# Kernel tuning notes

Hardware: AMD Instinct MI355X
Metric: run time of the kernel (lower is better)

The kernel has to match this reference:

```python
import jax, jax.numpy as jnp
import numpy as np

B, T, V, D, H, C = 128, 512, 50000, 128, 256, 10


def _lstm_scan(xs, W, U, b):
    # xs: [T, B, in]; Keras gate order i, f, g(candidate), o.
    xW = jnp.einsum('tbi,ij->tbj', xs, W) + b  # precompute input projection
    Bsz = xs.shape[1]
    Hd = U.shape[0]
    h0 = jnp.zeros((Bsz, Hd), xs.dtype)

    def step(carry, zx):
        h, c = carry
        z = zx + h @ U
        i, f, g, o = jnp.split(z, 4, axis=-1)
        i = jax.nn.sigmoid(i)
        f = jax.nn.sigmoid(f)
        g = jnp.tanh(g)
        o = jax.nn.sigmoid(o)
        c = f * c + i * g
        h = o * jnp.tanh(c)
        return (h, c), h

    (hT, _), hs = jax.lax.scan(step, (h0, h0), xW)
    return hs, hT


def setup_inputs() -> dict:
    key = jax.random.key(0)
    ks = jax.random.split(key, 16)
    f32 = jnp.float32

    def glorot(k, shape):
        fan = shape[0] + shape[1]
        return jax.random.uniform(k, shape, f32, -1.0, 1.0) * np.sqrt(6.0 / fan)

    x = jax.random.randint(ks[0], (B, T), 0, V, dtype=jnp.int32)
    emb = jax.random.normal(ks[1], (V, D), f32) * 0.05
    # layer 1: input D -> 4H per direction
    W1f = glorot(ks[2], (D, 4 * H)); U1f = glorot(ks[3], (H, 4 * H)); b1f = jnp.zeros((4 * H,), f32)
    W1b = glorot(ks[4], (D, 4 * H)); U1b = glorot(ks[5], (H, 4 * H)); b1b = jnp.zeros((4 * H,), f32)
    # layer 2: input 2H -> 4H per direction
    W2f = glorot(ks[6], (2 * H, 4 * H)); U2f = glorot(ks[7], (H, 4 * H)); b2f = jnp.zeros((4 * H,), f32)
    W2b = glorot(ks[8], (2 * H, 4 * H)); U2b = glorot(ks[9], (H, 4 * H)); b2b = jnp.zeros((4 * H,), f32)
    Wd = glorot(ks[10], (2 * H, C)); bd = jnp.zeros((C,), f32)
    return dict(x=x, emb=emb, W1f=W1f, U1f=U1f, b1f=b1f, W1b=W1b, U1b=U1b, b1b=b1b,
                W2f=W2f, U2f=U2f, b2f=b2f, W2b=W2b, U2b=U2b, b2b=b2b, Wd=Wd, bd=bd)


def reference(x, emb, W1f, U1f, b1f, W1b, U1b, b1b, W2f, U2f, b2f, W2b, U2b, b2b, Wd, bd):
    # Embedding lookup -> [T, B, D] (time-major for scan). Dropout is inference-off.
    e = jnp.transpose(emb[x], (1, 0, 2))
    # Bidirectional LSTM 1 (return_sequences)
    hs_f, _ = _lstm_scan(e, W1f, U1f, b1f)
    hs_b, _ = _lstm_scan(e[::-1], W1b, U1b, b1b)
    seq = jnp.concatenate([hs_f, hs_b[::-1]], axis=-1)  # [T, B, 2H]
    # Bidirectional LSTM 2 (return last states)
    _, hT_f = _lstm_scan(seq, W2f, U2f, b2f)
    _, hT_b = _lstm_scan(seq[::-1], W2b, U2b, b2b)
    h = jnp.concatenate([hT_f, hT_b], axis=-1)  # [B, 2H]
    return jax.nn.softmax(h @ Wd + bd, axis=-1)
```

## Files before the change

kernel.cpp:

```cpp
#include <hip/hip_runtime.h>
#include <hip/hip_bf16.h>

#define B_ 128
#define T_ 512
#define H_ 256
#define G4_ 1024
#define D_ 128

typedef short s8v   __attribute__((ext_vector_type(8)));
typedef float f32x4 __attribute__((ext_vector_type(4)));
typedef unsigned short u16x4 __attribute__((ext_vector_type(4)));
typedef unsigned short u16x8 __attribute__((ext_vector_type(8)));
typedef unsigned int   u32x4 __attribute__((ext_vector_type(4)));
typedef unsigned short ush;
typedef unsigned long long ull;

__device__ __align__(256) ush   g_xw[(size_t)T_ * 2 * B_ * G4_];
__device__ __align__(256) ush   g_hseq[(size_t)T_ * B_ * 512];
__device__ __align__(256) ull   g_hx2[8 * 2 * 2 * 256 * 8];
__device__ __align__(256) float g_hT[B_ * 512];
__device__ __align__(256) ush   g_wtall[2359296];

__device__ __forceinline__ ush f2b(float f) {
  unsigned u = __builtin_bit_cast(unsigned, f);
  u += 0x7FFFu + ((u >> 16) & 1u);
  return (ush)(u >> 16);
}
__device__ __forceinline__ float b2f(ush h) {
  unsigned u = ((unsigned)h) << 16;
  return __builtin_bit_cast(float, u);
}
__device__ __forceinline__ float sigm(float x) {
  x = fminf(15.f, fmaxf(-15.f, x));
  return 1.f / (1.f + __expf(-x));
}
__device__ __forceinline__ float tanh_(float x) {
  x = fminf(8.f, fmaxf(-8.f, x));
  float e = __expf(-2.f * x);
  return (1.f - e) / (1.f + e);
}

__global__ __launch_bounds__(256, 4) void prep_w(
    const float* __restrict__ Wf, const float* __restrict__ Wb,
    ush* __restrict__ WTf, ush* __restrict__ WTb, int K)
{
  __shared__ ush tile[64][65];
  const float* W = blockIdx.z ? Wb : Wf;
  ush* WT = blockIdx.z ? WTb : WTf;
  int nt = blockIdx.x & 15, kt = blockIdx.x >> 4;
  int tid = threadIdx.x;
  for (int i = tid; i < 4096; i += 256) {
    int k = i >> 6, n = i & 63;
    tile[k][n] = f2b(W[(size_t)(kt * 64 + k) * 1024 + nt * 64 + n]);
  }
  __syncthreads();
  for (int i = tid; i < 4096; i += 256) {
    int n = i >> 6, k = i & 63;
    WT[(size_t)(nt * 64 + n) * K + kt * 64 + k] = tile[k][n];
  }
}

__global__ __launch_bounds__(512, 4) void gemm_xw(
    int mode, const int* __restrict__ xi, const float* __restrict__ emb,
    const ush* __restrict__ WTf, const ush* __restrict__ WTb, int ktot)
{
  __shared__ __align__(16) ush A_lds[128 * 72];
  __shared__ __align__(16) ush BT_lds[128 * 72];
  const int tid = threadIdx.x;
  const int lane = tid & 63;
  const int w = tid >> 6;
  const int nb = blockIdx.x;
  const int t = blockIdx.y;
  const int dir = blockIdx.z;
  const ush* WT = dir ? WTb : WTf;

  const f32x4 zero4 = {0.f, 0.f, 0.f, 0.f};
  f32x4 acc[8];
#pragma unroll
  for (int i = 0; i < 8; ++i) acc[i] = zero4;

  const int rowA0 = tid >> 3;
  const int ccA = tid & 7;
  int idx0 = 0, idx1 = 0;
  if (mode == 0) {
    idx0 = xi[rowA0 * T_ + t];
    idx1 = xi[(rowA0 + 64) * T_ + t];
  }

  const int nch = ktot >> 6;
  for (int kc = 0; kc < nch; ++kc) {
    __syncthreads();
    if (mode == 0) {
      {
        const float* s = emb + (size_t)idx0 * D_ + kc * 64 + ccA * 8;
        f32x4 a = *(const f32x4*)s;
        f32x4 b = *(const f32x4*)(s + 4);
        u16x8 v;
        v[0]=f2b(a[0]); v[1]=f2b(a[1]); v[2]=f2b(a[2]); v[3]=f2b(a[3]);
        v[4]=f2b(b[0]); v[5]=f2b(b[1]); v[6]=f2b(b[2]); v[7]=f2b(b[3]);
        *(u16x8*)&A_lds[rowA0 * 72 + ccA * 8] = v;
      }
      {
        const float* s = emb + (size_t)idx1 * D_ + kc * 64 + ccA * 8;
        f32x4 a = *(const f32x4*)s;
        f32x4 b = *(const f32x4*)(s + 4);
        u16x8 v;
        v[0]=f2b(a[0]); v[1]=f2b(a[1]); v[2]=f2b(a[2]); v[3]=f2b(a[3]);
        v[4]=f2b(b[0]); v[5]=f2b(b[1]); v[6]=f2b(b[2]); v[7]=f2b(b[3]);
        *(u16x8*)&A_lds[(rowA0 + 64) * 72 + ccA * 8] = v;
      }
    } else {
      {
        const ush* s = g_hseq + ((size_t)(t * B_ + rowA0)) * 512 + kc * 64 + ccA * 8;
        *(u32x4*)&A_lds[rowA0 * 72 + ccA * 8] = *(const u32x4*)s;
      }
      {
        const ush* s = g_hseq + ((size_t)(t * B_ + rowA0 + 64)) * 512 + kc * 64 + ccA * 8;
        *(u32x4*)&A_lds[(rowA0 + 64) * 72 + ccA * 8] = *(const u32x4*)s;
      }
    }
    {
      int n = tid >> 2, k8 = (tid & 3) * 2;
      const ush* src = WT + (size_t)(nb * 128 + n) * ktot + kc * 64 + k8 * 8;
      *(u32x4*)&BT_lds[n * 72 + k8 * 8] = *(const u32x4*)src;
      *(u32x4*)&BT_lds[n * 72 + k8 * 8 + 8] = *(const u32x4*)(src + 8);
    }
    __syncthreads();
#pragma unroll
    for (int kt = 0; kt < 2; ++kt) {
      const int koff = kt * 32 + ((lane >> 4) << 3);
      s8v af = *(const s8v*)&A_lds[(w * 16 + (lane & 15)) * 72 + koff];
#pragma unroll
      for (int nt = 0; nt < 8; ++nt) {
        s8v bf = *(const s8v*)&BT_lds[(nt * 16 + (lane & 15)) * 72 + koff];
        acc[nt] = __builtin_amdgcn_mfma_f32_16x16x32_bf16(af, bf, acc[nt], 0, 0, 0);
      }
    }
  }
  ush* dst = g_xw + ((size_t)t * 2 + dir) * ((size_t)B_ * G4_);
#pragma unroll
  for (int nt = 0; nt < 8; ++nt) {
    int colg = nb * 128 + nt * 16 + (lane & 15);
    int g = colg >> 8, hc = colg & 255;
#pragma unroll
    for (int jj = 0; jj < 4; ++jj) {
      int row = w * 16 + ((lane >> 4) << 2) + jj;
      dst[(size_t)row * 1024 + hc * 4 + g] = f2b(acc[nt][jj]);
    }
  }
}

__global__ __launch_bounds__(512, 2) void lstm_rec(
    int layer, const ush* __restrict__ UTf, const ush* __restrict__ UTb,
    const float* __restrict__ bfp, const float* __restrict__ bbp,
    int writeSeq)
{
  __shared__ __align__(16) ush h_lds[2][16 * 256];

  const int tid = threadIdx.x;
  const int lane = tid & 63;
  const int w = tid >> 6;
  const int dir = blockIdx.x >> 4;
  const int nh = (blockIdx.x >> 3) & 1;
  const int slice = blockIdx.x & 7;
  const ush* UT = dir ? UTb : UTf;
  const float* bias = dir ? bbp : bfp;

  const int l15 = lane & 15;
  const int lq = lane >> 4;
  const int mycol = nh * 128 + w * 16 + l15;
  const int rowb = slice * 16;
  const unsigned sbase = (unsigned)(layer * T_);

  s8v bfr[4][8];
#pragma unroll
  for (int g = 0; g < 4; ++g) {
    const ush* up = UT + (size_t)(g * 256 + mycol) * 256;
#pragma unroll
    for (int kt = 0; kt < 8; ++kt)
      bfr[g][kt] = *(const s8v*)(up + kt * 32 + lq * 8);
  }
  float bias_r[4];
#pragma unroll
  for (int g = 0; g < 4; ++g) bias_r[g] = bias[g * 256 + mycol];

  {
    ull* z = (ull*)&h_lds[0][0];
    for (int i = tid; i < 1024; i += 512) z[i] = 0ull;
  }
  __syncthreads();

  float c_[4] = {0.f, 0.f, 0.f, 0.f};
  ull* hxp = g_hx2 + ((size_t)(slice * 2 + dir) * 2) * (256 * 8);

  const int colp = (nh ^ 1) * 128 + (tid >> 2);
  const int q = tid & 3;
  const int c8p = colp >> 3, wp = colp & 7;

  u16x4 xv[4];
  {
    int t0 = dir ? (T_ - 1) : 0;
    const ush* xp = g_xw + (((size_t)t0 * 2 + dir) * B_ + rowb) * 1024 + mycol * 4;
#pragma unroll
    for (int j = 0; j < 4; ++j)
      xv[j] = *(const u16x4*)(xp + (size_t)(lq * 4 + j) * 1024);
  }

  for (int s = 0; s < T_; ++s) {
    const int p = s & 1;

    if (s > 0) {
      const ull* a0 = hxp + ((size_t)p * 256 + colp) * 8 + q * 2;
      unsigned target = sbase + (unsigned)s;
      ull v0, v1;
      for (;;) {
        v0 = __hip_atomic_load(a0, __ATOMIC_RELAXED, __HIP_MEMORY_SCOPE_SYSTEM);
        v1 = __hip_atomic_load(a0 + 1, __ATOMIC_RELAXED, __HIP_MEMORY_SCOPE_SYSTEM);
        if ((unsigned)(v0 >> 32) >= target && (unsigned)(v1 >> 32) >= target) break;
        __builtin_amdgcn_s_sleep(1);
      }
      ush* dstl = &h_lds[p][0];
      dstl[(q * 4 + 0) * 256 + (((c8p ^ (q * 4 + 0)) & 31) * 8 + wp)] = (ush)v0;
      dstl[(q * 4 + 1) * 256 + (((c8p ^ (q * 4 + 1)) & 31) * 8 + wp)] = (ush)(v0 >> 16);
      dstl[(q * 4 + 2) * 256 + (((c8p ^ (q * 4 + 2)) & 31) * 8 + wp)] = (ush)v1;
      dstl[(q * 4 + 3) * 256 + (((c8p ^ (q * 4 + 3)) & 31) * 8 + wp)] = (ush)(v1 >> 16);
    }
    __syncthreads();

    if (writeSeq && s > 0 && tid < 256) {
      int row = tid >> 4, idx = tid & 15;
      int col = nh * 128 + idx * 8;
      int c8 = col >> 3;
      u32x4 hval = *(const u32x4*)&h_lds[p][row * 256 + ((c8 ^ row) & 31) * 8];
      int tprev = dir ? (T_ - s) : (s - 1);
      *(u32x4*)&g_hseq[((size_t)tprev * B_ + rowb + row) * 512 + dir * 256 + col] = hval;
    }

    s8v af[8];
#pragma unroll
    for (int kt = 0; kt < 8; ++kt) {
      int c8 = kt * 4 + lq;
      af[kt] = *(const s8v*)&h_lds[p][l15 * 256 + ((c8 ^ l15) & 31) * 8];
    }
    f32x4 acc[4];
    const f32x4 zero4 = {0.f, 0.f, 0.f, 0.f};
#pragma unroll
    for (int g = 0; g < 4; ++g) acc[g] = zero4;
#pragma unroll
    for (int kt = 0; kt < 8; ++kt) {
#pragma unroll
      for (int g = 0; g < 4; ++g)
        acc[g] = __builtin_amdgcn_mfma_f32_16x16x32_bf16(af[kt], bfr[g][kt], acc[g], 0, 0, 0);
    }
    float hf[4];
    ush hv[4];
#pragma unroll
    for (int j = 0; j < 4; ++j) {
      float vi = acc[0][j] + b2f(xv[j][0]) + bias_r[0];
      float vf = acc[1][j] + b2f(xv[j][1]) + bias_r[1];
      float vg = acc[2][j] + b2f(xv[j][2]) + bias_r[2];
      float vo = acc[3][j] + b2f(xv[j][3]) + bias_r[3];
      float ig = sigm(vi), fg = sigm(vf), gg = tanh_(vg), og = sigm(vo);
      float cc = fg * c_[j] + ig * gg;
      c_[j] = cc;
      hf[j] = og * tanh_(cc);
      hv[j] = f2b(hf[j]);
    }
    {
      ull seqw = ((ull)(sbase + (unsigned)s + 1u)) << 32;
      ull e0 = (ull)hv[0] | ((ull)hv[1] << 16) | seqw;
      ull e1 = (ull)hv[2] | ((ull)hv[3] << 16) | seqw;
      ull* ep = hxp + ((size_t)(p ^ 1) * 256 + mycol) * 8 + lq * 2;
      __hip_atomic_store(ep, e0, __ATOMIC_RELAXED, __HIP_MEMORY_SCOPE_SYSTEM);
      __hip_atomic_store(ep + 1, e1, __ATOMIC_RELAXED, __HIP_MEMORY_SCOPE_SYSTEM);
    }
    {
      int c8o = mycol >> 3, wo = mycol & 7;
#pragma unroll
      for (int j = 0; j < 4; ++j) {
        int row = lq * 4 + j;
        h_lds[p ^ 1][row * 256 + (((c8o ^ row) & 31) * 8 + wo)] = hv[j];
      }
    }
    if (s + 1 < T_) {
      int tn = dir ? (T_ - 2 - s) : (s + 1);
      const ush* xp = g_xw + (((size_t)tn * 2 + dir) * B_ + rowb) * 1024 + mycol * 4;
#pragma unroll
      for (int j = 0; j < 4; ++j)
        xv[j] = *(const u16x4*)(xp + (size_t)(lq * 4 + j) * 1024);
    }
  }

  {
    const ull* a0 = hxp + ((size_t)(T_ & 1) * 256 + colp) * 8 + q * 2;
    unsigned target = sbase + (unsigned)T_;
    ull v0, v1;
    for (;;) {
      v0 = __hip_atomic_load(a0, __ATOMIC_RELAXED, __HIP_MEMORY_SCOPE_SYSTEM);
      v1 = __hip_atomic_load(a0 + 1, __ATOMIC_RELAXED, __HIP_MEMORY_SCOPE_SYSTEM);
      if ((unsigned)(v0 >> 32) >= target && (unsigned)(v1 >> 32) >= target) break;
      __builtin_amdgcn_s_sleep(1);
    }
    ush* dstl = &h_lds[T_ & 1][0];
    dstl[(q * 4 + 0) * 256 + (((c8p ^ (q * 4 + 0)) & 31) * 8 + wp)] = (ush)v0;
    dstl[(q * 4 + 1) * 256 + (((c8p ^ (q * 4 + 1)) & 31) * 8 + wp)] = (ush)(v0 >> 16);
    dstl[(q * 4 + 2) * 256 + (((c8p ^ (q * 4 + 2)) & 31) * 8 + wp)] = (ush)v1;
    dstl[(q * 4 + 3) * 256 + (((c8p ^ (q * 4 + 3)) & 31) * 8 + wp)] = (ush)(v1 >> 16);
  }
  __syncthreads();
  if (tid < 256) {
    int row = tid >> 4, idx = tid & 15;
    int col = nh * 128 + idx * 8;
    int c8 = col >> 3;
    u32x4 hval = *(const u32x4*)&h_lds[T_ & 1][row * 256 + ((c8 ^ row) & 31) * 8];
    if (writeSeq) {
      int tprev = dir ? 0 : (T_ - 1);
      *(u32x4*)&g_hseq[((size_t)tprev * B_ + rowb + row) * 512 + dir * 256 + col] = hval;
    } else {
      const ush* hp = (const ush*)&hval;
      float* dstf = g_hT + (size_t)(rowb + row) * 512 + dir * 256 + col;
      f32x4 f0, f1;
#pragma unroll
      for (int j = 0; j < 4; ++j) { f0[j] = b2f(hp[j]); f1[j] = b2f(hp[4 + j]); }
      *(f32x4*)dstf = f0;
      *(f32x4*)(dstf + 4) = f1;
    }
  }
}

__global__ __launch_bounds__(512, 1) void dense_softmax(
    const float* __restrict__ Wd, const float* __restrict__ bd, float* __restrict__ out)
{
  __shared__ float wT[10 * 512];
  __shared__ float part[512 * 10];
  int tid = threadIdx.x;
  for (int i = tid; i < 5120; i += 512) {
    int k = i / 10, j = i - k * 10;
    wT[j * 512 + k] = Wd[i];
  }
  __syncthreads();
  int row = tid >> 2, q = tid & 3;
  float acc[10];
#pragma unroll
  for (int j = 0; j < 10; ++j) acc[j] = 0.f;
  const float* hrow = g_hT + (size_t)row * 512 + q * 128;
  for (int kk = 0; kk < 32; ++kk) {
    f32x4 h4 = *(const f32x4*)(hrow + kk * 4);
#pragma unroll
    for (int j = 0; j < 10; ++j) {
      f32x4 w4 = *(const f32x4*)&wT[j * 512 + q * 128 + kk * 4];
      acc[j] += h4[0] * w4[0] + h4[1] * w4[1] + h4[2] * w4[2] + h4[3] * w4[3];
    }
  }
#pragma unroll
  for (int j = 0; j < 10; ++j) part[tid * 10 + j] = acc[j];
  __syncthreads();
  if (tid < 128) {
    float lg[10];
#pragma unroll
    for (int j = 0; j < 10; ++j)
      lg[j] = bd[j] + part[(tid * 4 + 0) * 10 + j] + part[(tid * 4 + 1) * 10 + j]
                    + part[(tid * 4 + 2) * 10 + j] + part[(tid * 4 + 3) * 10 + j];
    float m = lg[0];
#pragma unroll
    for (int j = 1; j < 10; ++j) m = fmaxf(m, lg[j]);
    float ssum = 0.f;
#pragma unroll
    for (int j = 0; j < 10; ++j) { lg[j] = __expf(lg[j] - m); ssum += lg[j]; }
    float inv = 1.f / ssum;
#pragma unroll
    for (int j = 0; j < 10; ++j) out[tid * 10 + j] = lg[j] * inv;
  }
}

extern "C" void kernel_launch(void* const* d_in, const int* in_sizes, int n_in,
                              void* d_out, int out_size, void* d_ws, size_t ws_size,
                              hipStream_t stream) {
  (void)in_sizes; (void)n_in; (void)d_ws; (void)ws_size; (void)out_size;
  const int* x = (const int*)d_in[0];
  const float* emb = (const float*)d_in[1];
  const float* W1f = (const float*)d_in[2];
  const float* U1f = (const float*)d_in[3];
  const float* b1f = (const float*)d_in[4];
  const float* W1b = (const float*)d_in[5];
  const float* U1b = (const float*)d_in[6];
  const float* b1b = (const float*)d_in[7];
  const float* W2f = (const float*)d_in[8];
  const float* U2f = (const float*)d_in[9];
  const float* b2f = (const float*)d_in[10];
  const float* W2b = (const float*)d_in[11];
  const float* U2b = (const float*)d_in[12];
  const float* b2b = (const float*)d_in[13];
  const float* Wd  = (const float*)d_in[14];
  const float* bd  = (const float*)d_in[15];
  float* out = (float*)d_out;

  void* hx_p = nullptr; void* wt_p = nullptr;
  hipGetSymbolAddress(&hx_p, HIP_SYMBOL(g_hx2));
  hipGetSymbolAddress(&wt_p, HIP_SYMBOL(g_wtall));
  ush* wt = (ush*)wt_p;
  hipMemsetAsync(hx_p, 0, sizeof(ull) * 8 * 2 * 2 * 256 * 8, stream);

  ush* wt1f = wt;                 ush* wt1b = wt1f + 131072;
  ush* ut1f = wt1b + 131072;      ush* ut1b = ut1f + 262144;
  ush* wt2f = ut1b + 262144;      ush* wt2b = wt2f + 524288;
  ush* ut2f = wt2b + 524288;      ush* ut2b = ut2f + 262144;

  prep_w<<<dim3(32, 1, 2), 256, 0, stream>>>(W1f, W1b, wt1f, wt1b, 128);
  prep_w<<<dim3(64, 1, 2), 256, 0, stream>>>(U1f, U1b, ut1f, ut1b, 256);
  prep_w<<<dim3(128, 1, 2), 256, 0, stream>>>(W2f, W2b, wt2f, wt2b, 512);
  prep_w<<<dim3(64, 1, 2), 256, 0, stream>>>(U2f, U2b, ut2f, ut2b, 256);

  gemm_xw<<<dim3(8, T_, 2), 512, 0, stream>>>(0, x, emb, wt1f, wt1b, 128);
  lstm_rec<<<32, 512, 0, stream>>>(0, ut1f, ut1b, b1f, b1b, 1);
  gemm_xw<<<dim3(8, T_, 2), 512, 0, stream>>>(1, nullptr, nullptr, wt2f, wt2b, 512);
  lstm_rec<<<32, 512, 0, stream>>>(1, ut2f, ut2b, b2f, b2b, 0);
  dense_softmax<<<1, 512, 0, stream>>>(Wd, bd, out);
}
```

Measured before the change: 3.872 ms.

## Fuse layer-2 input GEMM into layer-1 recurrence via per-timestep readiness counters

The layer-1 recurrent kernel becomes a persistent mega-kernel. 64 blocks run the LSTM recurrence, now split into 16 batch slices of 8 rows instead of 8 slices of 16, giving twice as many recurrent blocks. The remaining 160 blocks compute the layer-2 input projection GEMM as soon as per-timestep counters show both directions have written that timestep's hidden state. This hides the layer-2 xW GEMM under the latency-bound layer-1 scan and removes a separate kernel launch. In exchange it adds atomic counters, spin-waiting, and a co-residency assumption: GEMM blocks must not starve the recurrent blocks.

```diff
diff --git a/kernel.cpp b/kernel.cpp
--- a/kernel.cpp
+++ b/kernel.cpp
@@ -17,8 +17,9 @@
 
 __device__ __align__(256) ush   g_xw[(size_t)T_ * 2 * B_ * G4_];
 __device__ __align__(256) ush   g_hseq[(size_t)T_ * B_ * 512];
-__device__ __align__(256) ull   g_hx2[8 * 2 * 2 * 256 * 8];
+__device__ __align__(256) ull   g_hx2[16 * 2 * 2 * 256 * 4];
 __device__ __align__(256) float g_hT[B_ * 512];
+__device__ __align__(256) unsigned g_tcnt[512];
 __device__ __align__(256) ush   g_wtall[2359296];
 
 __device__ __forceinline__ ush f2b(float f) {
@@ -61,8 +62,8 @@
 }
 
 __global__ __launch_bounds__(512, 4) void gemm_xw(
-    int mode, const int* __restrict__ xi, const float* __restrict__ emb,
-    const ush* __restrict__ WTf, const ush* __restrict__ WTb, int ktot)
+    const int* __restrict__ xi, const float* __restrict__ emb,
+    const ush* __restrict__ WTf, const ush* __restrict__ WTb)
 {
   __shared__ __align__(16) ush A_lds[128 * 72];
   __shared__ __align__(16) ush BT_lds[128 * 72];
@@ -81,47 +82,32 @@
 
   const int rowA0 = tid >> 3;
   const int ccA = tid & 7;
-  int idx0 = 0, idx1 = 0;
-  if (mode == 0) {
-    idx0 = xi[rowA0 * T_ + t];
-    idx1 = xi[(rowA0 + 64) * T_ + t];
-  }
-
-  const int nch = ktot >> 6;
-  for (int kc = 0; kc < nch; ++kc) {
+  int idx0 = xi[rowA0 * T_ + t];
+  int idx1 = xi[(rowA0 + 64) * T_ + t];
+
+  for (int kc = 0; kc < 2; ++kc) {
     __syncthreads();
-    if (mode == 0) {
-      {
-        const float* s = emb + (size_t)idx0 * D_ + kc * 64 + ccA * 8;
-        f32x4 a = *(const f32x4*)s;
-        f32x4 b = *(const f32x4*)(s + 4);
-        u16x8 v;
-        v[0]=f2b(a[0]); v[1]=f2b(a[1]); v[2]=f2b(a[2]); v[3]=f2b(a[3]);
-        v[4]=f2b(b[0]); v[5]=f2b(b[1]); v[6]=f2b(b[2]); v[7]=f2b(b[3]);
-        *(u16x8*)&A_lds[rowA0 * 72 + ccA * 8] = v;
-      }
-      {
-        const float* s = emb + (size_t)idx1 * D_ + kc * 64 + ccA * 8;
-        f32x4 a = *(const f32x4*)s;
-        f32x4 b = *(const f32x4*)(s + 4);
-        u16x8 v;
-        v[0]=f2b(a[0]); v[1]=f2b(a[1]); v[2]=f2b(a[2]); v[3]=f2b(a[3]);
-        v[4]=f2b(b[0]); v[5]=f2b(b[1]); v[6]=f2b(b[2]); v[7]=f2b(b[3]);
-        *(u16x8*)&A_lds[(rowA0 + 64) * 72 + ccA * 8] = v;
-      }
-    } else {
-      {
-        const ush* s = g_hseq + ((size_t)(t * B_ + rowA0)) * 512 + kc * 64 + ccA * 8;
-        *(u32x4*)&A_lds[rowA0 * 72 + ccA * 8] = *(const u32x4*)s;
-      }
-      {
-        const ush* s = g_hseq + ((size_t)(t * B_ + rowA0 + 64)) * 512 + kc * 64 + ccA * 8;
-        *(u32x4*)&A_lds[(rowA0 + 64) * 72 + ccA * 8] = *(const u32x4*)s;
-      }
+    {
+      const float* s = emb + (size_t)idx0 * D_ + kc * 64 + ccA * 8;
+      f32x4 a = *(const f32x4*)s;
+      f32x4 b = *(const f32x4*)(s + 4);
+      u16x8 v;
+      v[0]=f2b(a[0]); v[1]=f2b(a[1]); v[2]=f2b(a[2]); v[3]=f2b(a[3]);
+      v[4]=f2b(b[0]); v[5]=f2b(b[1]); v[6]=f2b(b[2]); v[7]=f2b(b[3]);
+      *(u16x8*)&A_lds[rowA0 * 72 + ccA * 8] = v;
+    }
+    {
+      const float* s = emb + (size_t)idx1 * D_ + kc * 64 + ccA * 8;
+      f32x4 a = *(const f32x4*)s;
+      f32x4 b = *(const f32x4*)(s + 4);
+      u16x8 v;
+      v[0]=f2b(a[0]); v[1]=f2b(a[1]); v[2]=f2b(a[2]); v[3]=f2b(a[3]);
+      v[4]=f2b(b[0]); v[5]=f2b(b[1]); v[6]=f2b(b[2]); v[7]=f2b(b[3]);
+      *(u16x8*)&A_lds[(rowA0 + 64) * 72 + ccA * 8] = v;
     }
     {
       int n = tid >> 2, k8 = (tid & 3) * 2;
-      const ush* src = WT + (size_t)(nb * 128 + n) * ktot + kc * 64 + k8 * 8;
+      const ush* src = WT + (size_t)(nb * 128 + n) * 128 + kc * 64 + k8 * 8;
       *(u32x4*)&BT_lds[n * 72 + k8 * 8] = *(const u32x4*)src;
       *(u32x4*)&BT_lds[n * 72 + k8 * 8 + 8] = *(const u32x4*)(src + 8);
     }
@@ -150,180 +136,251 @@
   }
 }
 
-__global__ __launch_bounds__(512, 2) void lstm_rec(
+__global__ __launch_bounds__(512, 2) void mega(
     int layer, const ush* __restrict__ UTf, const ush* __restrict__ UTb,
     const float* __restrict__ bfp, const float* __restrict__ bbp,
-    int writeSeq)
+    int writeSeq, int ngemm,
+    const ush* __restrict__ WT2f, const ush* __restrict__ WT2b)
 {
-  __shared__ __align__(16) ush h_lds[2][16 * 256];
-
+  __shared__ __align__(16) ush smem[2 * 128 * 72];
+  const int bx = blockIdx.x;
   const int tid = threadIdx.x;
   const int lane = tid & 63;
   const int w = tid >> 6;
-  const int dir = blockIdx.x >> 4;
-  const int nh = (blockIdx.x >> 3) & 1;
-  const int slice = blockIdx.x & 7;
-  const ush* UT = dir ? UTb : UTf;
-  const float* bias = dir ? bbp : bfp;
-
   const int l15 = lane & 15;
   const int lq = lane >> 4;
-  const int mycol = nh * 128 + w * 16 + l15;
-  const int rowb = slice * 16;
-  const unsigned sbase = (unsigned)(layer * T_);
-
-  s8v bfr[4][8];
-#pragma unroll
-  for (int g = 0; g < 4; ++g) {
-    const ush* up = UT + (size_t)(g * 256 + mycol) * 256;
-#pragma unroll
-    for (int kt = 0; kt < 8; ++kt)
-      bfr[g][kt] = *(const s8v*)(up + kt * 32 + lq * 8);
-  }
-  float bias_r[4];
-#pragma unroll
-  for (int g = 0; g < 4; ++g) bias_r[g] = bias[g * 256 + mycol];
-
-  {
-    ull* z = (ull*)&h_lds[0][0];
-    for (int i = tid; i < 1024; i += 512) z[i] = 0ull;
-  }
-  __syncthreads();
-
-  float c_[4] = {0.f, 0.f, 0.f, 0.f};
-  ull* hxp = g_hx2 + ((size_t)(slice * 2 + dir) * 2) * (256 * 8);
-
-  const int colp = (nh ^ 1) * 128 + (tid >> 2);
-  const int q = tid & 3;
-  const int c8p = colp >> 3, wp = colp & 7;
-
-  u16x4 xv[4];
-  {
-    int t0 = dir ? (T_ - 1) : 0;
-    const ush* xp = g_xw + (((size_t)t0 * 2 + dir) * B_ + rowb) * 1024 + mycol * 4;
-#pragma unroll
-    for (int j = 0; j < 4; ++j)
-      xv[j] = *(const u16x4*)(xp + (size_t)(lq * 4 + j) * 1024);
-  }
-
-  for (int s = 0; s < T_; ++s) {
-    const int p = s & 1;
-
-    if (s > 0) {
-      const ull* a0 = hxp + ((size_t)p * 256 + colp) * 8 + q * 2;
-      unsigned target = sbase + (unsigned)s;
-      ull v0, v1;
+
+  if (bx < 64) {
+    const int slice = bx & 15;
+    const int dir = (bx >> 4) & 1;
+    const int nh = bx >> 5;
+    const ush* UT = dir ? UTb : UTf;
+    const float* bias = dir ? bbp : bfp;
+    const int mycol = nh * 128 + w * 16 + l15;
+    const int rowb = slice * 8;
+    const unsigned sbase = (unsigned)(layer * T_);
+    ush* h0 = smem;
+
+    s8v bfr[4][8];
+#pragma unroll
+    for (int g = 0; g < 4; ++g) {
+      const ush* up = UT + (size_t)(g * 256 + mycol) * 256;
+#pragma unroll
+      for (int kt = 0; kt < 8; ++kt)
+        bfr[g][kt] = *(const s8v*)(up + kt * 32 + lq * 8);
+    }
+    float bias_r[4];
+#pragma unroll
+    for (int g = 0; g < 4; ++g) bias_r[g] = bias[g * 256 + mycol];
+
+    {
+      ull* z = (ull*)smem;
+      z[tid] = 0ull; z[tid + 512] = 0ull; z[tid + 1024] = 0ull; z[tid + 1536] = 0ull;
+    }
+    __syncthreads();
+
+    float c_[4] = {0.f, 0.f, 0.f, 0.f};
+    ull* hx_base = g_hx2 + (size_t)(slice * 2 + dir) * 2048;
+    const int colp = (nh ^ 1) * 128 + (tid >> 2);
+    const int m_ = tid & 3;
+    const int c8p = colp >> 3, wp = colp & 7;
+    const int xrow = (lq & 1) * 4;
+
+    u16x4 xv[4];
+    {
+      int t0 = dir ? (T_ - 1) : 0;
+      const ush* xp = g_xw + (((size_t)t0 * 2 + dir) * B_ + rowb) * 1024 + mycol * 4;
+#pragma unroll
+      for (int j = 0; j < 4; ++j) xv[j] = *(const u16x4*)(xp + (size_t)(xrow + j) * 1024);
+    }
+
+    for (int s = 0; s < T_; ++s) {
+      const int p = s & 1;
+      if (s > 0) {
+        ull* aP = hx_base + ((size_t)p * 256 + colp) * 4 + m_;
+        unsigned target = sbase + (unsigned)s;
+        ull v;
+        for (;;) {
+          v = __hip_atomic_load(aP, __ATOMIC_RELAXED, __HIP_MEMORY_SCOPE_SYSTEM);
+          if ((unsigned)(v >> 32) >= target) break;
+          __builtin_amdgcn_s_sleep(1);
+        }
+        int r0 = 2 * m_;
+        ush* dl = h0 + p * 4096;
+        dl[r0 * 256 + (((c8p ^ r0) & 31) * 8 + wp)] = (ush)v;
+        dl[(r0 + 1) * 256 + (((c8p ^ (r0 + 1)) & 31) * 8 + wp)] = (ush)(v >> 16);
+      }
+      __syncthreads();
+      if (writeSeq) {
+        if (tid == 0 && s >= 2) {
+          int td = dir ? (T_ + 1 - s) : (s - 2);
+          __hip_atomic_fetch_add(&g_tcnt[td], 1u, __ATOMIC_RELAXED, __HIP_MEMORY_SCOPE_SYSTEM);
+        }
+        if (s > 0 && tid < 128) {
+          int row8 = tid >> 4, idx = tid & 15;
+          int col = nh * 128 + idx * 8;
+          int c8 = col >> 3;
+          const ush* srcl = h0 + p * 4096 + row8 * 256 + ((c8 ^ row8) & 31) * 8;
+          ull lo = *(const ull*)srcl;
+          ull hi = *(const ull*)(srcl + 4);
+          int tprev = dir ? (T_ - s) : (s - 1);
+          ull* dst = (ull*)&g_hseq[((size_t)tprev * B_ + rowb + row8) * 512 + dir * 256 + col];
+          __hip_atomic_store(dst, lo, __ATOMIC_RELAXED, __HIP_MEMORY_SCOPE_SYSTEM);
+          __hip_atomic_store(dst + 1, hi, __ATOMIC_RELAXED, __HIP_MEMORY_SCOPE_SYSTEM);
+        }
+      }
+      u16x4 xn[4];
+      if (s + 1 < T_) {
+        int tn = dir ? (T_ - 2 - s) : (s + 1);
+        const ush* xp = g_xw + (((size_t)tn * 2 + dir) * B_ + rowb) * 1024 + mycol * 4;
+#pragma unroll
+        for (int j = 0; j < 4; ++j) xn[j] = *(const u16x4*)(xp + (size_t)(xrow + j) * 1024);
+      }
+      s8v af[8];
+#pragma unroll
+      for (int kt = 0; kt < 8; ++kt) {
+        int c8 = kt * 4 + lq;
+        af[kt] = *(const s8v*)(h0 + p * 4096 + l15 * 256 + ((c8 ^ l15) & 31) * 8);
+      }
+      f32x4 acc[4];
+      const f32x4 zero4 = {0.f, 0.f, 0.f, 0.f};
+#pragma unroll
+      for (int g = 0; g < 4; ++g) acc[g] = zero4;
+#pragma unroll
+      for (int kt = 0; kt < 8; ++kt) {
+#pragma unroll
+        for (int g = 0; g < 4; ++g)
+          acc[g] = __builtin_amdgcn_mfma_f32_16x16x32_bf16(af[kt], bfr[g][kt], acc[g], 0, 0, 0);
+      }
+      float hf[4];
+      ush hv[4];
+#pragma unroll
+      for (int j = 0; j < 4; ++j) {
+        float vi = acc[0][j] + b2f(xv[j][0]) + bias_r[0];
+        float vf = acc[1][j] + b2f(xv[j][1]) + bias_r[1];
+        float vg = acc[2][j] + b2f(xv[j][2]) + bias_r[2];
+        float vo = acc[3][j] + b2f(xv[j][3]) + bias_r[3];
+        float ig = sigm(vi), fg = sigm(vf), gg = tanh_(vg), og = sigm(vo);
+        float cc = fg * c_[j] + ig * gg;
+        c_[j] = cc;
+        hf[j] = og * tanh_(cc);
+        hv[j] = f2b(hf[j]);
+      }
+      (void)hf;
+      if (lq < 2) {
+        ull seqw = ((ull)(sbase + (unsigned)s + 1u)) << 32;
+        ull e0 = (ull)hv[0] | ((ull)hv[1] << 16) | seqw;
+        ull e1 = (ull)hv[2] | ((ull)hv[3] << 16) | seqw;
+        ull* ep = hx_base + ((size_t)(p ^ 1) * 256 + mycol) * 4 + 2 * lq;
+        __hip_atomic_store(ep, e0, __ATOMIC_RELAXED, __HIP_MEMORY_SCOPE_SYSTEM);
+        __hip_atomic_store(ep + 1, e1, __ATOMIC_RELAXED, __HIP_MEMORY_SCOPE_SYSTEM);
+        int c8o = mycol >> 3, wo = mycol & 7;
+        ush* dl = h0 + (p ^ 1) * 4096;
+#pragma unroll
+        for (int j = 0; j < 4; ++j) {
+          int r = lq * 4 + j;
+          dl[r * 256 + (((c8o ^ r) & 31) * 8 + wo)] = hv[j];
+        }
+      }
+#pragma unroll
+      for (int j = 0; j < 4; ++j) xv[j] = xn[j];
+    }
+    __syncthreads();
+    const ush* bufl = h0 + (T_ & 1) * 4096;
+    if (writeSeq) {
+      if (tid < 128) {
+        int row8 = tid >> 4, idx = tid & 15;
+        int col = nh * 128 + idx * 8;
+        int c8 = col >> 3;
+        const ush* srcl = bufl + row8 * 256 + ((c8 ^ row8) & 31) * 8;
+        ull lo = *(const ull*)srcl;
+        ull hi = *(const ull*)(srcl + 4);
+        int tlast = dir ? 0 : (T_ - 1);
+        ull* dst = (ull*)&g_hseq[((size_t)tlast * B_ + rowb + row8) * 512 + dir * 256 + col];
+        __hip_atomic_store(dst, lo, __ATOMIC_RELAXED, __HIP_MEMORY_SCOPE_SYSTEM);
+        __hip_atomic_store(dst + 1, hi, __ATOMIC_RELAXED, __HIP_MEMORY_SCOPE_SYSTEM);
+      }
+      asm volatile("s_waitcnt vmcnt(0)" ::: "memory");
+      __syncthreads();
+      if (tid == 0) {
+        int ta = dir ? 1 : (T_ - 2);
+        int tb2 = dir ? 0 : (T_ - 1);
+        __hip_atomic_fetch_add(&g_tcnt[ta], 1u, __ATOMIC_RELAXED, __HIP_MEMORY_SCOPE_SYSTEM);
+        __hip_atomic_fetch_add(&g_tcnt[tb2], 1u, __ATOMIC_RELAXED, __HIP_MEMORY_SCOPE_SYSTEM);
+      }
+    } else {
+      if (tid < 128) {
+        int row8 = tid >> 4, idx = tid & 15;
+        int col = nh * 128 + idx * 8;
+        int c8 = col >> 3;
+        const ush* srcl = bufl + row8 * 256 + ((c8 ^ row8) & 31) * 8;
+        float* dstf = g_hT + (size_t)(rowb + row8) * 512 + dir * 256 + col;
+        f32x4 f0, f1;
+#pragma unroll
+        for (int j = 0; j < 4; ++j) { f0[j] = b2f(srcl[j]); f1[j] = b2f(srcl[4 + j]); }
+        *(f32x4*)dstf = f0;
+        *(f32x4*)(dstf + 4) = f1;
+      }
+    }
+  } else {
+    if (ngemm <= 0) return;
+    ush* A_lds = smem;
+    ush* BT_lds = smem + 128 * 72;
+    const int wg = bx - 64;
+    const int rowA0 = tid >> 3;
+    const int ccA = tid & 7;
+
+    for (int u = wg; u < 8192; u += ngemm) {
+      int pairIdx = u >> 4, sub = u & 15;
+      int nb = sub & 7, gdir = sub >> 3;
+      int t = (pairIdx & 1) ? (255 - (pairIdx >> 1)) : (256 + (pairIdx >> 1));
+      const ush* WT = gdir ? WT2b : WT2f;
       for (;;) {
-        v0 = __hip_atomic_load(a0, __ATOMIC_RELAXED, __HIP_MEMORY_SCOPE_SYSTEM);
-        v1 = __hip_atomic_load(a0 + 1, __ATOMIC_RELAXED, __HIP_MEMORY_SCOPE_SYSTEM);
-        if ((unsigned)(v0 >> 32) >= target && (unsigned)(v1 >> 32) >= target) break;
-        __builtin_amdgcn_s_sleep(1);
-      }
-      ush* dstl = &h_lds[p][0];
-      dstl[(q * 4 + 0) * 256 + (((c8p ^ (q * 4 + 0)) & 31) * 8 + wp)] = (ush)v0;
-      dstl[(q * 4 + 1) * 256 + (((c8p ^ (q * 4 + 1)) & 31) * 8 + wp)] = (ush)(v0 >> 16);
-      dstl[(q * 4 + 2) * 256 + (((c8p ^ (q * 4 + 2)) & 31) * 8 + wp)] = (ush)v1;
-      dstl[(q * 4 + 3) * 256 + (((c8p ^ (q * 4 + 3)) & 31) * 8 + wp)] = (ush)(v1 >> 16);
-    }
-    __syncthreads();
-
-    if (writeSeq && s > 0 && tid < 256) {
-      int row = tid >> 4, idx = tid & 15;
-      int col = nh * 128 + idx * 8;
-      int c8 = col >> 3;
-      u32x4 hval = *(const u32x4*)&h_lds[p][row * 256 + ((c8 ^ row) & 31) * 8];
-      int tprev = dir ? (T_ - s) : (s - 1);
-      *(u32x4*)&g_hseq[((size_t)tprev * B_ + rowb + row) * 512 + dir * 256 + col] = hval;
-    }
-
-    s8v af[8];
-#pragma unroll
-    for (int kt = 0; kt < 8; ++kt) {
-      int c8 = kt * 4 + lq;
-      af[kt] = *(const s8v*)&h_lds[p][l15 * 256 + ((c8 ^ l15) & 31) * 8];
-    }
-    f32x4 acc[4];
-    const f32x4 zero4 = {0.f, 0.f, 0.f, 0.f};
-#pragma unroll
-    for (int g = 0; g < 4; ++g) acc[g] = zero4;
-#pragma unroll
-    for (int kt = 0; kt < 8; ++kt) {
-#pragma unroll
-      for (int g = 0; g < 4; ++g)
-        acc[g] = __builtin_amdgcn_mfma_f32_16x16x32_bf16(af[kt], bfr[g][kt], acc[g], 0, 0, 0);
-    }
-    float hf[4];
-    ush hv[4];
-#pragma unroll
-    for (int j = 0; j < 4; ++j) {
-      float vi = acc[0][j] + b2f(xv[j][0]) + bias_r[0];
-      float vf = acc[1][j] + b2f(xv[j][1]) + bias_r[1];
-      float vg = acc[2][j] + b2f(xv[j][2]) + bias_r[2];
-      float vo = acc[3][j] + b2f(xv[j][3]) + bias_r[3];
-      float ig = sigm(vi), fg = sigm(vf), gg = tanh_(vg), og = sigm(vo);
-      float cc = fg * c_[j] + ig * gg;
-      c_[j] = cc;
-      hf[j] = og * tanh_(cc);
-      hv[j] = f2b(hf[j]);
-    }
-    {
-      ull seqw = ((ull)(sbase + (unsigned)s + 1u)) << 32;
-      ull e0 = (ull)hv[0] | ((ull)hv[1] << 16) | seqw;
-      ull e1 = (ull)hv[2] | ((ull)hv[3] << 16) | seqw;
-      ull* ep = hxp + ((size_t)(p ^ 1) * 256 + mycol) * 8 + lq * 2;
-      __hip_atomic_store(ep, e0, __ATOMIC_RELAXED, __HIP_MEMORY_SCOPE_SYSTEM);
-      __hip_atomic_store(ep + 1, e1, __ATOMIC_RELAXED, __HIP_MEMORY_SCOPE_SYSTEM);
-    }
-    {
-      int c8o = mycol >> 3, wo = mycol & 7;
-#pragma unroll
-      for (int j = 0; j < 4; ++j) {
-        int row = lq * 4 + j;
-        h_lds[p ^ 1][row * 256 + (((c8o ^ row) & 31) * 8 + wo)] = hv[j];
-      }
-    }
-    if (s + 1 < T_) {
-      int tn = dir ? (T_ - 2 - s) : (s + 1);
-      const ush* xp = g_xw + (((size_t)tn * 2 + dir) * B_ + rowb) * 1024 + mycol * 4;
-#pragma unroll
-      for (int j = 0; j < 4; ++j)
-        xv[j] = *(const u16x4*)(xp + (size_t)(lq * 4 + j) * 1024);
-    }
-  }
-
-  {
-    const ull* a0 = hxp + ((size_t)(T_ & 1) * 256 + colp) * 8 + q * 2;
-    unsigned target = sbase + (unsigned)T_;
-    ull v0, v1;
-    for (;;) {
-      v0 = __hip_atomic_load(a0, __ATOMIC_RELAXED, __HIP_MEMORY_SCOPE_SYSTEM);
-      v1 = __hip_atomic_load(a0 + 1, __ATOMIC_RELAXED, __HIP_MEMORY_SCOPE_SYSTEM);
-      if ((unsigned)(v0 >> 32) >= target && (unsigned)(v1 >> 32) >= target) break;
-      __builtin_amdgcn_s_sleep(1);
-    }
-    ush* dstl = &h_lds[T_ & 1][0];
-    dstl[(q * 4 + 0) * 256 + (((c8p ^ (q * 4 + 0)) & 31) * 8 + wp)] = (ush)v0;
-    dstl[(q * 4 + 1) * 256 + (((c8p ^ (q * 4 + 1)) & 31) * 8 + wp)] = (ush)(v0 >> 16);
-    dstl[(q * 4 + 2) * 256 + (((c8p ^ (q * 4 + 2)) & 31) * 8 + wp)] = (ush)v1;
-    dstl[(q * 4 + 3) * 256 + (((c8p ^ (q * 4 + 3)) & 31) * 8 + wp)] = (ush)(v1 >> 16);
-  }
-  __syncthreads();
-  if (tid < 256) {
-    int row = tid >> 4, idx = tid & 15;
-    int col = nh * 128 + idx * 8;
-    int c8 = col >> 3;
-    u32x4 hval = *(const u32x4*)&h_lds[T_ & 1][row * 256 + ((c8 ^ row) & 31) * 8];
-    if (writeSeq) {
-      int tprev = dir ? 0 : (T_ - 1);
-      *(u32x4*)&g_hseq[((size_t)tprev * B_ + rowb + row) * 512 + dir * 256 + col] = hval;
-    } else {
-      const ush* hp = (const ush*)&hval;
-      float* dstf = g_hT + (size_t)(rowb + row) * 512 + dir * 256 + col;
-      f32x4 f0, f1;
-#pragma unroll
-      for (int j = 0; j < 4; ++j) { f0[j] = b2f(hp[j]); f1[j] = b2f(hp[4 + j]); }
-      *(f32x4*)dstf = f0;
-      *(f32x4*)(dstf + 4) = f1;
+        unsigned v = __hip_atomic_load(&g_tcnt[t], __ATOMIC_RELAXED, __HIP_MEMORY_SCOPE_SYSTEM);
+        if (v >= 64u) break;
+        __builtin_amdgcn_s_sleep(4);
+      }
+      const f32x4 zero4 = {0.f, 0.f, 0.f, 0.f};
+      f32x4 acc[8];
+#pragma unroll
+      for (int i = 0; i < 8; ++i) acc[i] = zero4;
+      for (int kc = 0; kc < 8; ++kc) {
+        __syncthreads();
+        {
+          const ush* s0 = g_hseq + ((size_t)(t * B_ + rowA0)) * 512 + kc * 64 + ccA * 8;
+          *(u32x4*)&A_lds[rowA0 * 72 + ccA * 8] = *(const u32x4*)s0;
+          const ush* s1 = g_hseq + ((size_t)(t * B_ + rowA0 + 64)) * 512 + kc * 64 + ccA * 8;
+          *(u32x4*)&A_lds[(rowA0 + 64) * 72 + ccA * 8] = *(const u32x4*)s1;
+        }
+        {
+          int n = tid >> 2, k8 = (tid & 3) * 2;
+          const ush* src = WT + (size_t)(nb * 128 + n) * 512 + kc * 64 + k8 * 8;
+          *(u32x4*)&BT_lds[n * 72 + k8 * 8] = *(const u32x4*)src;
+          *(u32x4*)&BT_lds[n * 72 + k8 * 8 + 8] = *(const u32x4*)(src + 8);
+        }
+        __syncthreads();
+#pragma unroll
+        for (int kt = 0; kt < 2; ++kt) {
+          const int koff = kt * 32 + (lq << 3);
+          s8v af = *(const s8v*)&A_lds[(w * 16 + l15) * 72 + koff];
+#pragma unroll
+          for (int nt = 0; nt < 8; ++nt) {
+            s8v bf = *(const s8v*)&BT_lds[(nt * 16 + l15) * 72 + koff];
+            acc[nt] = __builtin_amdgcn_mfma_f32_16x16x32_bf16(af, bf, acc[nt], 0, 0, 0);
+          }
+        }
+      }
+      ush* dst = g_xw + ((size_t)t * 2 + gdir) * ((size_t)B_ * G4_);
+#pragma unroll
+      for (int nt = 0; nt < 8; ++nt) {
+        int colg = nb * 128 + nt * 16 + l15;
+        int g = colg >> 8, hc = colg & 255;
+#pragma unroll
+        for (int jj = 0; jj < 4; ++jj) {
+          int row = w * 16 + (lq << 2) + jj;
+          dst[(size_t)row * 1024 + hc * 4 + g] = f2b(acc[nt][jj]);
+        }
+      }
     }
   }
 }
@@ -395,11 +452,13 @@
   const float* bd  = (const float*)d_in[15];
   float* out = (float*)d_out;
 
-  void* hx_p = nullptr; void* wt_p = nullptr;
+  void* hx_p = nullptr; void* wt_p = nullptr; void* tc_p = nullptr;
   hipGetSymbolAddress(&hx_p, HIP_SYMBOL(g_hx2));
   hipGetSymbolAddress(&wt_p, HIP_SYMBOL(g_wtall));
+  hipGetSymbolAddress(&tc_p, HIP_SYMBOL(g_tcnt));
   ush* wt = (ush*)wt_p;
-  hipMemsetAsync(hx_p, 0, sizeof(ull) * 8 * 2 * 2 * 256 * 8, stream);
+  hipMemsetAsync(hx_p, 0, sizeof(ull) * 16 * 2 * 2 * 256 * 4, stream);
+  hipMemsetAsync(tc_p, 0, sizeof(unsigned) * 512, stream);
 
   ush* wt1f = wt;                 ush* wt1b = wt1f + 131072;
   ush* ut1f = wt1b + 131072;      ush* ut1b = ut1f + 262144;
@@ -411,9 +470,8 @@
   prep_w<<<dim3(128, 1, 2), 256, 0, stream>>>(W2f, W2b, wt2f, wt2b, 512);
   prep_w<<<dim3(64, 1, 2), 256, 0, stream>>>(U2f, U2b, ut2f, ut2b, 256);
 
-  gemm_xw<<<dim3(8, T_, 2), 512, 0, stream>>>(0, x, emb, wt1f, wt1b, 128);
-  lstm_rec<<<32, 512, 0, stream>>>(0, ut1f, ut1b, b1f, b1b, 1);
-  gemm_xw<<<dim3(8, T_, 2), 512, 0, stream>>>(1, nullptr, nullptr, wt2f, wt2b, 512);
-  lstm_rec<<<32, 512, 0, stream>>>(1, ut2f, ut2b, b2f, b2b, 0);
+  gemm_xw<<<dim3(8, T_, 2), 512, 0, stream>>>(x, emb, wt1f, wt1b);
+  mega<<<224, 512, 0, stream>>>(0, ut1f, ut1b, b1f, b1b, 1, 160, wt2f, wt2b);
+  mega<<<64, 512, 0, stream>>>(1, ut2f, ut2b, b2f, b2b, 0, 0, nullptr, nullptr);
   dense_softmax<<<1, 512, 0, stream>>>(Wd, bd, out);
 }
```

After: 3.788 ms. -2.2%, faster.
